# Kernel tuning notes

Measured on AMD Instinct MI355X. Metric: run time of the kernel, lower is better.

## Reference

```python
import jax, jax.numpy as jnp
import numpy as np

D_MODEL = 1024
N_HEADS = 16
D_HEAD = D_MODEL // N_HEADS
ROPE_BASE = 10000.0
B, L = 2, 2048


def setup_inputs() -> dict:
    key = jax.random.key(0)
    k1, k2, k3 = jax.random.split(key, 3)
    x = jax.random.normal(k1, (B, L, D_MODEL), dtype=jnp.float32)
    W_qkv = jax.random.normal(k2, (3 * D_MODEL, D_MODEL), dtype=jnp.float32) * (1.0 / np.sqrt(D_MODEL))
    W_out = jax.random.normal(k3, (D_MODEL, D_MODEL), dtype=jnp.float32) * (1.0 / np.sqrt(D_MODEL))
    position_ids = jnp.broadcast_to(jnp.arange(L, dtype=jnp.int32), (B, L))
    attn_mask_2d = jnp.broadcast_to(jnp.tril(jnp.ones((L, L), dtype=bool)), (B, L, L))
    return {"x": x, "W_qkv": W_qkv, "W_out": W_out,
            "position_ids": position_ids, "attn_mask_2d": attn_mask_2d}


def _apply_rope(t, position_ids, inv_freq):
    # t: (B, H, L, Dh) float32; position_ids: (B, L) int
    f = position_ids.astype(jnp.float32)[:, :, None] * inv_freq  # (B, L, Dh/2)
    cos = jnp.cos(f)[:, None]  # (B, 1, L, Dh/2)
    sin = jnp.sin(f)[:, None]
    x1 = t[..., 0::2]
    x2 = t[..., 1::2]
    rot_even = x1 * cos - x2 * sin
    rot_odd = x1 * sin + x2 * cos
    return jnp.stack((rot_even, rot_odd), axis=-1).reshape(t.shape)


def reference(x, W_qkv, W_out, position_ids, attn_mask_2d):
    Bb, Ll, D = x.shape
    H, Dh = N_HEADS, D // N_HEADS
    inv_freq = 1.0 / (ROPE_BASE ** (jnp.arange(0, Dh, 2, dtype=jnp.float32) / Dh))  # (Dh/2,)
    qkv = jnp.einsum('bld,ed->ble', x, W_qkv).reshape(Bb, Ll, 3, H, Dh)
    qkv = jnp.transpose(qkv, (2, 0, 3, 1, 4))  # (3, B, H, L, Dh)
    q, k, v = qkv[0], qkv[1], qkv[2]
    q = _apply_rope(q.astype(jnp.float32), position_ids, inv_freq).astype(x.dtype)
    k = _apply_rope(k.astype(jnp.float32), position_ids, inv_freq).astype(x.dtype)
    scale = 1.0 / np.sqrt(Dh).astype(np.float32)
    scores = jnp.einsum('bhld,bhmd->bhlm', q, k) * scale  # (B, H, L, L)
    neg = jnp.finfo(scores.dtype).min
    scores = jnp.where(attn_mask_2d[:, None], scores, neg)
    attn = jax.nn.softmax(scores, axis=-1)
    out = jnp.einsum('bhlm,bhmd->bhld', attn, v)
    out = jnp.transpose(out, (0, 2, 1, 3)).reshape(Bb, Ll, D)
    return jnp.einsum('bld,ed->ble', out, W_out)
```

## Files before the change

kernel.cpp:

```cpp
#include <hip/hip_runtime.h>
#include <hip/hip_bf16.h>
#include <math.h>

typedef float f32x4 __attribute__((ext_vector_type(4)));
typedef __bf16 bf16x8 __attribute__((ext_vector_type(8)));

__device__ inline f32x4 mfma16(bf16x8 a, bf16x8 b, f32x4 c) {
    return __builtin_amdgcn_mfma_f32_16x16x32_bf16(a, b, c, 0, 0, 0);
}
__device__ inline unsigned short f2bf(float f) {
    union { float f; unsigned u; } v; v.f = f;
    unsigned r = v.u + 0x7fffu + ((v.u >> 16) & 1u);
    return (unsigned short)(r >> 16);
}
__device__ inline float bf2f(unsigned short b) {
    union { unsigned u; float f; } v; v.u = ((unsigned)b) << 16;
    return v.f;
}
__device__ inline unsigned pack2(float a, float b) {
    return (unsigned)f2bf(a) | ((unsigned)f2bf(b) << 16);
}
__device__ inline f32x4 vzero() { f32x4 z = {0.f, 0.f, 0.f, 0.f}; return z; }

#define GLD16(gptr, lptr)                                                            \
    __builtin_amdgcn_global_load_lds(                                                \
        (const __attribute__((address_space(1))) unsigned int*)(const void*)(gptr),  \
        (__attribute__((address_space(3))) unsigned int*)(void*)(lptr), 16, 0, 0)

__global__ __launch_bounds__(256)
void convert_xw(const float* __restrict__ x, const float* __restrict__ wqkv,
                unsigned short* __restrict__ xb, unsigned short* __restrict__ wqkvb)
{
    int i = blockIdx.x * 256 + threadIdx.x;
    const float* src; unsigned short* dst; int off;
    if (i < 524288) { src = x;    dst = xb;    off = i; }
    else            { src = wqkv; dst = wqkvb; off = i - 524288; }
    const float4* p = (const float4*)src + (size_t)off * 2;
    float4 f0 = p[0], f1 = p[1];
    uint4 o;
    o.x = pack2(f0.x, f0.y); o.y = pack2(f0.z, f0.w);
    o.z = pack2(f1.x, f1.y); o.w = pack2(f1.z, f1.w);
    ((uint4*)dst)[off] = o;
}

template<int MI, int C32, int WPB>
__global__ __launch_bounds__(256, WPB)
void gemm_bt(const unsigned short* __restrict__ A,
             const unsigned short* __restrict__ Wt,
             void* __restrict__ C_, int M, int N, int K)
{
    __shared__ __align__(16) unsigned short As[MI * 32 * 64];
    __shared__ __align__(16) unsigned short Bs[128 * 64];

    const int tid  = threadIdx.x;
    const int wave = tid >> 6;
    const int lane = tid & 63;
    const int quad = lane >> 4;
    const int c0   = lane & 15;
    const int m0 = blockIdx.y * (MI * 32);
    const int n0 = blockIdx.x * 128;
    const int wm = (wave >> 1) * (MI * 16);
    const int wn = (wave & 1) * 64;

    const int lrow   = lane >> 3;
    const int gchunk = (lane & 7) ^ lrow;
    const int goff   = gchunk * 8;

    f32x4 acc[MI][4];
#pragma unroll
    for (int i = 0; i < MI; i++)
#pragma unroll
        for (int j = 0; j < 4; j++) acc[i][j] = vzero();

    for (int k0 = 0; k0 < K; k0 += 64) {
        __syncthreads();
#pragma unroll
        for (int p = 0; p < MI; p++) {
            int r0 = p * 32 + wave * 8;
            GLD16(&A[(size_t)(m0 + r0 + lrow) * K + k0 + goff], &As[r0 * 64]);
        }
#pragma unroll
        for (int p = 0; p < 4; p++) {
            int r0 = p * 32 + wave * 8;
            GLD16(&Wt[(size_t)(n0 + r0 + lrow) * K + k0 + goff], &Bs[r0 * 64]);
        }
        __syncthreads();
#pragma unroll
        for (int kk = 0; kk < 2; kk++) {
            const int pos = ((kk * 4 + quad) ^ (c0 & 7)) * 8;
            bf16x8 af[MI], bfr[4];
#pragma unroll
            for (int i = 0; i < MI; i++)
                af[i] = *(const bf16x8*)&As[(wm + i * 16 + c0) * 64 + pos];
#pragma unroll
            for (int j = 0; j < 4; j++)
                bfr[j] = *(const bf16x8*)&Bs[(wn + j * 16 + c0) * 64 + pos];
#pragma unroll
            for (int i = 0; i < MI; i++)
#pragma unroll
                for (int j = 0; j < 4; j++)
                    acc[i][j] = mfma16(af[i], bfr[j], acc[i][j]);
        }
    }

#pragma unroll
    for (int i = 0; i < MI; i++)
#pragma unroll
        for (int j = 0; j < 4; j++)
#pragma unroll
            for (int r = 0; r < 4; r++) {
                int row  = m0 + wm + i * 16 + quad * 4 + r;
                int colg = n0 + wn + j * 16 + c0;
                if (C32) ((float*)C_)[(size_t)row * N + colg] = acc[i][j][r];
                else ((unsigned short*)C_)[(size_t)row * N + colg] = f2bf(acc[i][j][r]);
            }
}

__global__ __launch_bounds__(256)
void rope_vtrans(const unsigned short* __restrict__ qkv,
                 const int* __restrict__ pos,
                 unsigned short* __restrict__ Qb,
                 unsigned short* __restrict__ Kb,
                 unsigned short* __restrict__ Vt,
                 const float* __restrict__ wout,
                 unsigned short* __restrict__ woutb)
{
    __shared__ unsigned short T[256 * 64];
    const int id = blockIdx.x;
    if (id < 8192) {
        int tid = id * 256 + threadIdx.x;
        int d2 = tid & 31;
        int h  = (tid >> 5) & 15;
        int l  = (tid >> 9) & 2047;
        int b  = tid >> 20;
        size_t row = (size_t)(b * 2048 + l) * 3072;
        int col = h * 64 + 2 * d2;
        float inv_freq = exp2f((float)(-2 * d2) * (13.287712379549449f / 64.0f));
        float f = (float)pos[b * 2048 + l] * inv_freq;
        float s, c;
        sincosf(f, &s, &c);
        unsigned qw = *(const unsigned*)&qkv[row + col];
        unsigned kw = *(const unsigned*)&qkv[row + 1024 + col];
        float q1 = bf2f((unsigned short)qw), q2 = bf2f((unsigned short)(qw >> 16));
        float k1 = bf2f((unsigned short)kw), k2 = bf2f((unsigned short)(kw >> 16));
        const float qs = 0.18033688011112042f;
        size_t o = ((size_t)((b * 16 + h) * 2048 + l)) * 64 + 2 * d2;
        *(unsigned*)&Qb[o] = pack2((q1 * c - q2 * s) * qs, (q1 * s + q2 * c) * qs);
        *(unsigned*)&Kb[o] = pack2(k1 * c - k2 * s, k1 * s + k2 * c);
    } else if (id < 8448) {
        const int id2 = id - 8192;
        const int t = threadIdx.x;
        const int l0 = (id2 & 7) * 256, h = (id2 >> 3) & 15, b = id2 >> 7;
#pragma unroll
        for (int i = 0; i < 8; i++) {
            int c = t + i * 256;
            int r = c >> 3, c8 = c & 7;
            int p = (c8 + (r >> 3)) & 7;
            *(uint4*)&T[r * 64 + p * 8] =
                *(const uint4*)&qkv[(size_t)(b * 2048 + l0 + r) * 3072 + 2048 + h * 64 + c8 * 8];
        }
        __syncthreads();
#pragma unroll
        for (int i = 0; i < 8; i++) {
            int c = t + i * 256;
            int dh = c >> 5, lc = c & 31;
            int blk = dh >> 3;
            unsigned short tmp[8];
#pragma unroll
            for (int j = 0; j < 8; j++) {
                int l = lc * 8 + j;
                int p = (blk + lc) & 7;
                tmp[j] = T[l * 64 + p * 8 + (dh & 7)];
            }
            *(uint4*)&Vt[((size_t)(b * 16 + h) * 64 + dh) * 2048 + l0 + lc * 8] = *(uint4*)tmp;
        }
    } else {
        int i = (id - 8448) * 256 + threadIdx.x;
        const float4* p = (const float4*)wout + (size_t)i * 2;
        float4 f0 = p[0], f1 = p[1];
        uint4 o;
        o.x = pack2(f0.x, f0.y); o.y = pack2(f0.z, f0.w);
        o.z = pack2(f1.x, f1.y); o.w = pack2(f1.z, f1.w);
        ((uint4*)woutb)[i] = o;
    }
}

__global__ __launch_bounds__(256, 4)
void attn(const unsigned short* __restrict__ Q,
          const unsigned short* __restrict__ Kb,
          const unsigned short* __restrict__ Vt,
          unsigned short* __restrict__ O)
{
    __shared__ unsigned short Qs[64 * 64];
    __shared__ unsigned short Ks[64 * 64];
    __shared__ unsigned short Vts[64 * 64];
    __shared__ unsigned short Ps[64 * 64];

    const int tid  = threadIdx.x;
    const int wave = tid >> 6;
    const int lane = tid & 63;
    const int quad = lane >> 4;
    const int c0   = lane & 15;
    const int id = blockIdx.x;
    const int g  = id >> 5;
    const int gg = g & 7;
    const int gq = g >> 3;
    const int qt = (gq == 0) ? (31 - gg) : (gq == 1) ? gg
                 : (gq == 2) ? (23 - gg) : (8 + gg);
    const int h  = id & 15;
    const int b  = (id >> 4) & 1;
    const size_t headoff = ((size_t)(b * 16 + h)) * 2048 * 64;
    const int q0 = qt * 64;
    const float C = 11.541560327111707f;

    const int ca = tid, cb2 = tid + 256;
    const int ra = ca >> 3, c8a = ca & 7;
    const int rb = cb2 >> 3, c8b = cb2 & 7;
    const int la = ra * 64 + (c8a ^ (ra & 7)) * 8;
    const int lb = rb * 64 + (c8b ^ (rb & 7)) * 8;

    bf16x8 ones;
#pragma unroll
    for (int j = 0; j < 8; j++) ones[j] = (__bf16)1.0f;

    uint4 kreg0, kreg1, vreg0, vreg1;
    {
        kreg0 = *(const uint4*)&Kb[headoff + (size_t)ra * 64 + c8a * 8];
        kreg1 = *(const uint4*)&Kb[headoff + (size_t)rb * 64 + c8b * 8];
        vreg0 = *(const uint4*)&Vt[headoff + (size_t)ra * 2048 + c8a * 8];
        vreg1 = *(const uint4*)&Vt[headoff + (size_t)rb * 2048 + c8b * 8];
    }
    *(uint4*)&Qs[la] = *(const uint4*)&Q[headoff + (size_t)(q0 + ra) * 64 + c8a * 8];
    *(uint4*)&Qs[lb] = *(const uint4*)&Q[headoff + (size_t)(q0 + rb) * 64 + c8b * 8];

    f32x4 o[4];
#pragma unroll
    for (int j = 0; j < 4; j++) o[j] = vzero();
    f32x4 lacc = vzero();

    for (int kt = 0; kt <= qt; kt++) {
        __syncthreads();
        *(uint4*)&Ks[la] = kreg0;
        *(uint4*)&Ks[lb] = kreg1;
        *(uint4*)&Vts[la] = vreg0;
        *(uint4*)&Vts[lb] = vreg1;
        __syncthreads();
        if (kt < qt) {
            size_t k1o = headoff + (size_t)(kt + 1) * 4096;
            kreg0 = *(const uint4*)&Kb[k1o + (size_t)ra * 64 + c8a * 8];
            kreg1 = *(const uint4*)&Kb[k1o + (size_t)rb * 64 + c8b * 8];
            vreg0 = *(const uint4*)&Vt[headoff + (size_t)ra * 2048 + (kt + 1) * 64 + c8a * 8];
            vreg1 = *(const uint4*)&Vt[headoff + (size_t)rb * 2048 + (kt + 1) * 64 + c8b * 8];
        }

        {
            f32x4 s[4];
#pragma unroll
            for (int nj = 0; nj < 4; nj++) s[nj] = vzero();
#pragma unroll
            for (int kk = 0; kk < 2; kk++) {
                const int pos = ((kk * 4 + quad) ^ (c0 & 7)) * 8;
                bf16x8 aq = *(const bf16x8*)&Qs[(wave * 16 + c0) * 64 + pos];
#pragma unroll
                for (int nj = 0; nj < 4; nj++) {
                    bf16x8 bk = *(const bf16x8*)&Ks[(nj * 16 + c0) * 64 + pos];
                    s[nj] = mfma16(aq, bk, s[nj]);
                }
            }
            if (kt == qt) {
#pragma unroll
                for (int nj = 0; nj < 4; nj++)
#pragma unroll
                    for (int r = 0; r < 4; r++) {
                        int key  = nj * 16 + c0;
                        int qrow = wave * 16 + quad * 4 + r;
                        if (key > qrow) s[nj][r] = -1e38f;
                    }
            }
#pragma unroll
            for (int nj = 0; nj < 4; nj++)
#pragma unroll
                for (int r = 0; r < 4; r++) {
                    union { float f; unsigned u; } pv;
                    pv.f = __builtin_amdgcn_exp2f(s[nj][r] - C);
                    int row = wave * 16 + quad * 4 + r;
                    int col = nj * 16 + c0;
                    int pp = ((col >> 3) + row) & 7;
                    Ps[row * 64 + pp * 8 + (col & 7)] = (unsigned short)(pv.u >> 16);
                }
        }
        asm volatile("s_waitcnt lgkmcnt(0)" ::: "memory");

#pragma unroll
        for (int kk = 0; kk < 2; kk++) {
            const int pos = ((kk * 4 + quad) ^ (c0 & 7)) * 8;
            int prow = wave * 16 + c0;
            int pp = ((kk * 4 + quad) + prow) & 7;
            bf16x8 ap = *(const bf16x8*)&Ps[prow * 64 + pp * 8];
            lacc = mfma16(ap, ones, lacc);
#pragma unroll
            for (int cj = 0; cj < 4; cj++) {
                bf16x8 bv = *(const bf16x8*)&Vts[(cj * 16 + c0) * 64 + pos];
                o[cj] = mfma16(ap, bv, o[cj]);
            }
        }
    }

#pragma unroll
    for (int r = 0; r < 4; r++) {
        float inv = 1.0f / lacc[r];
        int ql = q0 + wave * 16 + quad * 4 + r;
        size_t base = ((size_t)b * 2048 + ql) * 1024 + h * 64;
#pragma unroll
        for (int cj = 0; cj < 4; cj++) {
            O[base + cj * 16 + c0] = f2bf(o[cj][r] * inv);
        }
    }
}

extern "C" void kernel_launch(void* const* d_in, const int* in_sizes, int n_in,
                              void* d_out, int out_size, void* d_ws, size_t ws_size,
                              hipStream_t stream) {
    const int* pos = (const int*)d_in[3];

    unsigned short* regA = (unsigned short*)d_ws;
    unsigned short* regB = regA + (size_t)4096 * 1024;
    unsigned short* regC = regB + (size_t)4096 * 1024;
    unsigned short* regD = regC + (size_t)4096 * 1024;
    unsigned short* regE = regD + (size_t)4096 * 3072;

    unsigned short* xb    = regA;
    unsigned short* wqkvb = regB;
    unsigned short* qkv   = regD;
    unsigned short* Qb    = regA;
    unsigned short* Kb    = regB;
    unsigned short* Vt    = regC;
    unsigned short* Ob    = regD;
    unsigned short* woutb = regE;

    convert_xw<<<3584, 256, 0, stream>>>((const float*)d_in[0], (const float*)d_in[1],
                                         xb, wqkvb);
    gemm_bt<4, 0, 4><<<dim3(24, 32), 256, 0, stream>>>(xb, wqkvb, qkv, 4096, 3072, 1024);
    rope_vtrans<<<8960, 256, 0, stream>>>(qkv, pos, Qb, Kb, Vt,
                                          (const float*)d_in[2], woutb);
    attn<<<1024, 256, 0, stream>>>(Qb, Kb, Vt, Ob);
    gemm_bt<2, 1, 3><<<dim3(8, 64), 256, 0, stream>>>(Ob, woutb, d_out, 4096, 1024, 1024);
}
```

Measured before the change: 201.6 us.

## Double-buffer K/V tiles in attention via direct global-to-LDS loads

Replaces the register-staged K/V prefetch with double-buffered LDS tiles filled by direct global-to-LDS loads (GLD16) one tile ahead, which removes one barrier per iteration. Q fragments are now held in registers instead of shared memory. s_setprio raises wave priority around the MFMA sections. LDS per block grows from 32KB to 40KB, which may affect occupancy at 4 blocks per CU, and correctness depends on the async LDS loads completing before the end-of-loop barrier.

```diff
diff --git a/kernel.cpp b/kernel.cpp
--- a/kernel.cpp
+++ b/kernel.cpp
@@ -191,9 +191,8 @@
           const unsigned short* __restrict__ Vt,
           unsigned short* __restrict__ O)
 {
-    __shared__ unsigned short Qs[64 * 64];
-    __shared__ unsigned short Ks[64 * 64];
-    __shared__ unsigned short Vts[64 * 64];
+    __shared__ unsigned short Ks[2][64 * 64];
+    __shared__ unsigned short Vts[2][64 * 64];
     __shared__ unsigned short Ps[64 * 64];
 
     const int tid  = threadIdx.x;
@@ -213,84 +212,82 @@
     const int q0 = qt * 64;
     const float C = 11.541560327111707f;
 
-    const int ca = tid, cb2 = tid + 256;
-    const int ra = ca >> 3, c8a = ca & 7;
-    const int rb = cb2 >> 3, c8b = cb2 & 7;
-    const int la = ra * 64 + (c8a ^ (ra & 7)) * 8;
-    const int lb = rb * 64 + (c8b ^ (rb & 7)) * 8;
+    const int lrow8 = lane >> 3;
+    const int goff  = ((lane & 7) ^ lrow8) * 8;
 
     bf16x8 ones;
 #pragma unroll
     for (int j = 0; j < 8; j++) ones[j] = (__bf16)1.0f;
 
-    uint4 kreg0, kreg1, vreg0, vreg1;
-    {
-        kreg0 = *(const uint4*)&Kb[headoff + (size_t)ra * 64 + c8a * 8];
-        kreg1 = *(const uint4*)&Kb[headoff + (size_t)rb * 64 + c8b * 8];
-        vreg0 = *(const uint4*)&Vt[headoff + (size_t)ra * 2048 + c8a * 8];
-        vreg1 = *(const uint4*)&Vt[headoff + (size_t)rb * 2048 + c8b * 8];
-    }
-    *(uint4*)&Qs[la] = *(const uint4*)&Q[headoff + (size_t)(q0 + ra) * 64 + c8a * 8];
-    *(uint4*)&Qs[lb] = *(const uint4*)&Q[headoff + (size_t)(q0 + rb) * 64 + c8b * 8];
+    auto stage = [&](int kt, int buf) {
+#pragma unroll
+        for (int i = 0; i < 2; i++) {
+            const int r0 = wave * 16 + i * 8;
+            const int r  = r0 + lrow8;
+            GLD16(&Kb[headoff + (size_t)kt * 4096 + (size_t)r * 64 + goff],
+                  &Ks[buf][r0 * 64]);
+            GLD16(&Vt[headoff + (size_t)r * 2048 + kt * 64 + goff],
+                  &Vts[buf][r0 * 64]);
+        }
+    };
+
+    stage(0, 0);
+    const size_t qbase = headoff + (size_t)(q0 + wave * 16 + c0) * 64;
+    bf16x8 aq0 = *(const bf16x8*)&Q[qbase + quad * 8];
+    bf16x8 aq1 = *(const bf16x8*)&Q[qbase + (4 + quad) * 8];
 
     f32x4 o[4];
 #pragma unroll
     for (int j = 0; j < 4; j++) o[j] = vzero();
     f32x4 lacc = vzero();
 
+    __syncthreads();
+
+    int cur = 0;
     for (int kt = 0; kt <= qt; kt++) {
-        __syncthreads();
-        *(uint4*)&Ks[la] = kreg0;
-        *(uint4*)&Ks[lb] = kreg1;
-        *(uint4*)&Vts[la] = vreg0;
-        *(uint4*)&Vts[lb] = vreg1;
-        __syncthreads();
-        if (kt < qt) {
-            size_t k1o = headoff + (size_t)(kt + 1) * 4096;
-            kreg0 = *(const uint4*)&Kb[k1o + (size_t)ra * 64 + c8a * 8];
-            kreg1 = *(const uint4*)&Kb[k1o + (size_t)rb * 64 + c8b * 8];
-            vreg0 = *(const uint4*)&Vt[headoff + (size_t)ra * 2048 + (kt + 1) * 64 + c8a * 8];
-            vreg1 = *(const uint4*)&Vt[headoff + (size_t)rb * 2048 + (kt + 1) * 64 + c8b * 8];
-        }
-
-        {
-            f32x4 s[4];
-#pragma unroll
-            for (int nj = 0; nj < 4; nj++) s[nj] = vzero();
-#pragma unroll
-            for (int kk = 0; kk < 2; kk++) {
-                const int pos = ((kk * 4 + quad) ^ (c0 & 7)) * 8;
-                bf16x8 aq = *(const bf16x8*)&Qs[(wave * 16 + c0) * 64 + pos];
-#pragma unroll
-                for (int nj = 0; nj < 4; nj++) {
-                    bf16x8 bk = *(const bf16x8*)&Ks[(nj * 16 + c0) * 64 + pos];
-                    s[nj] = mfma16(aq, bk, s[nj]);
+        if (kt < qt) stage(kt + 1, cur ^ 1);
+        const unsigned short* KsC  = Ks[cur];
+        const unsigned short* VtsC = Vts[cur];
+
+        f32x4 s[4];
+#pragma unroll
+        for (int nj = 0; nj < 4; nj++) s[nj] = vzero();
+        __builtin_amdgcn_s_setprio(1);
+#pragma unroll
+        for (int kk = 0; kk < 2; kk++) {
+            const int pos = ((kk * 4 + quad) ^ (c0 & 7)) * 8;
+            bf16x8 aq = kk ? aq1 : aq0;
+#pragma unroll
+            for (int nj = 0; nj < 4; nj++) {
+                bf16x8 bk = *(const bf16x8*)&KsC[(nj * 16 + c0) * 64 + pos];
+                s[nj] = mfma16(aq, bk, s[nj]);
+            }
+        }
+        __builtin_amdgcn_s_setprio(0);
+        if (kt == qt) {
+#pragma unroll
+            for (int nj = 0; nj < 4; nj++)
+#pragma unroll
+                for (int r = 0; r < 4; r++) {
+                    int key  = nj * 16 + c0;
+                    int qrow = wave * 16 + quad * 4 + r;
+                    if (key > qrow) s[nj][r] = -1e38f;
                 }
-            }
-            if (kt == qt) {
-#pragma unroll
-                for (int nj = 0; nj < 4; nj++)
-#pragma unroll
-                    for (int r = 0; r < 4; r++) {
-                        int key  = nj * 16 + c0;
-                        int qrow = wave * 16 + quad * 4 + r;
-                        if (key > qrow) s[nj][r] = -1e38f;
-                    }
-            }
-#pragma unroll
-            for (int nj = 0; nj < 4; nj++)
-#pragma unroll
-                for (int r = 0; r < 4; r++) {
-                    union { float f; unsigned u; } pv;
-                    pv.f = __builtin_amdgcn_exp2f(s[nj][r] - C);
-                    int row = wave * 16 + quad * 4 + r;
-                    int col = nj * 16 + c0;
-                    int pp = ((col >> 3) + row) & 7;
-                    Ps[row * 64 + pp * 8 + (col & 7)] = (unsigned short)(pv.u >> 16);
-                }
-        }
+        }
+#pragma unroll
+        for (int nj = 0; nj < 4; nj++)
+#pragma unroll
+            for (int r = 0; r < 4; r++) {
+                union { float f; unsigned u; } pv;
+                pv.f = __builtin_amdgcn_exp2f(s[nj][r] - C);
+                int row = wave * 16 + quad * 4 + r;
+                int col = nj * 16 + c0;
+                int pp = ((col >> 3) + row) & 7;
+                Ps[row * 64 + pp * 8 + (col & 7)] = (unsigned short)(pv.u >> 16);
+            }
         asm volatile("s_waitcnt lgkmcnt(0)" ::: "memory");
 
+        __builtin_amdgcn_s_setprio(1);
 #pragma unroll
         for (int kk = 0; kk < 2; kk++) {
             const int pos = ((kk * 4 + quad) ^ (c0 & 7)) * 8;
@@ -300,10 +297,14 @@
             lacc = mfma16(ap, ones, lacc);
 #pragma unroll
             for (int cj = 0; cj < 4; cj++) {
-                bf16x8 bv = *(const bf16x8*)&Vts[(cj * 16 + c0) * 64 + pos];
+                bf16x8 bv = *(const bf16x8*)&VtsC[(cj * 16 + c0) * 64 + pos];
                 o[cj] = mfma16(ap, bv, o[cj]);
             }
         }
+        __builtin_amdgcn_s_setprio(0);
+
+        __syncthreads();
+        cur ^= 1;
     }
 
 #pragma unroll
```

After: 207.4 us. 2.8% more time.
